# Kernel optimization log

Hardware: AMD Instinct MI355X
Metric: run time of the kernel (lower is better)

## Reference

```python
import jax, jax.numpy as jnp
import numpy as np

B, N, C_IN = 32, 4096, 32
C_OUT = 64
K = 5            # poly_degree
P = 4            # pooling_size
NNZ = 65536      # N * avg_degree(16)


def setup_inputs() -> dict:
    key = jax.random.key(0)
    ks = jax.random.split(key, 6)
    x = jax.random.normal(ks[0], (B, N, C_IN), dtype=jnp.float32)
    # scale edge values so the Chebyshev recursion stays numerically bounded
    edge_val = jax.random.normal(ks[1], (NNZ,), dtype=jnp.float32) * 0.05
    weight = jax.random.normal(ks[2], (K * C_IN, C_OUT), dtype=jnp.float32) * 0.1
    bias = jax.random.normal(ks[3], (1, 1, C_OUT), dtype=jnp.float32) * 0.1
    edge_row = jax.random.randint(ks[4], (NNZ,), 0, N, dtype=jnp.int32)
    edge_col = jax.random.randint(ks[5], (NNZ,), 0, N, dtype=jnp.int32)
    return {"x": x, "edge_val": edge_val, "weight": weight, "bias": bias,
            "edge_row": edge_row, "edge_col": edge_col}


def reference(x, edge_val, weight, bias, edge_row, edge_col):
    b, n, c = x.shape
    out_f = weight.shape[1]
    k_deg = weight.shape[0] // c

    def spmm(v):  # sparse (COO) L @ v, v: [n, c*b]
        gathered = v[edge_col] * edge_val[:, None]          # [nnz, c*b]
        return jax.ops.segment_sum(gathered, edge_row, num_segments=n)

    # x0: [n, c*b]
    x0 = jnp.transpose(x, (1, 2, 0)).reshape(n, c * b)
    x_list = [x0]
    if k_deg > 1:
        x1 = spmm(x0)
        x_list.append(x1)
    for _ in range(2, k_deg):
        x2 = 2.0 * spmm(x1) - x0
        x_list.append(x2)
        x0, x1 = x1, x2

    xs = jnp.stack(x_list, axis=0)                          # [K, n, c, b] after reshape
    xs = xs.reshape(k_deg, n, c, b)
    xs = jnp.transpose(xs, (3, 1, 2, 0))                    # [b, n, c, K]
    xs = xs.reshape(b * n, c * k_deg)
    y = (xs @ weight).reshape(b, n, out_f)                  # dense GEMM

    y = jax.nn.relu(y + bias)                               # bias + ReLU

    if P > 1:  # max pool of size P over node dim
        y = y.reshape(b, n // P, P, out_f).max(axis=2)
    return y
```

## Files before the change

kernel.cpp:

```cpp
#include <hip/hip_runtime.h>
#include <hip/hip_bf16.h>

#define BATCH 32
#define NNODE 4096
#define CIN 32
#define COUT 64
#define KDEG 5
#define POOL 4
#define NNZ_E 65536
#define BC (BATCH * CIN)
#define TBF ((size_t)NNODE * BC)
#define NSLICE 8

typedef short s16x8 __attribute__((ext_vector_type(8)));
typedef float f32x4 __attribute__((ext_vector_type(4)));
typedef unsigned long long u64;

__device__ __forceinline__ unsigned short f2bf(float f) {
    union { float f; unsigned int u; } v; v.f = f;
    unsigned int u = v.u;
    u += 0x7fffu + ((u >> 16) & 1u);
    return (unsigned short)(u >> 16);
}
__device__ __forceinline__ float bf2f(unsigned short b) {
    union { float f; unsigned int u; } v; v.u = ((unsigned int)b) << 16;
    return v.f;
}
__device__ __forceinline__ u64 pack4(float a, float b, float c, float d) {
    return (u64)f2bf(a) | ((u64)f2bf(b) << 16) | ((u64)f2bf(c) << 32) | ((u64)f2bf(d) << 48);
}


__global__ void prep_kernel(const float* __restrict__ x, unsigned short* __restrict__ t0,
                            const int* __restrict__ erow, int* __restrict__ cnt,
                            const float* __restrict__ W, unsigned short* __restrict__ WB) {
    int idx = blockIdx.x * 256 + threadIdx.x;
    int n   = idx >> 8;
    int rem = idx & 255;
    int b   = rem >> 3;
    int c4  = rem & 7;
    float4 v = ((const float4*)x)[(b * NNODE + n) * 8 + c4];
    ((u64*)t0)[idx] = pack4(v.x, v.y, v.z, v.w);

    if (idx < NNZ_E) atomicAdd(&cnt[erow[idx]], 1);

    if (idx < KDEG * COUT * CIN) {
        int c = idx & 31;
        int rest = idx >> 5;
        int o = rest & 63;
        int k = rest >> 6;
        WB[idx] = f2bf(W[(c * KDEG + k) * COUT + o]);
    }
}


__global__ void scan_kernel(const int* __restrict__ cnt, int* __restrict__ row_start,
                            int* __restrict__ cursor) {
    __shared__ int sums[256];
    int tid = threadIdx.x;
    int local[16];
    int s = 0;
#pragma unroll
    for (int i = 0; i < 16; i++) { local[i] = cnt[tid * 16 + i]; s += local[i]; }
    sums[tid] = s;
    __syncthreads();
    for (int off = 1; off < 256; off <<= 1) {
        int v = 0;
        if (tid >= off) v = sums[tid - off];
        __syncthreads();
        if (tid >= off) sums[tid] += v;
        __syncthreads();
    }
    int base = sums[tid] - s;
    int run = base;
#pragma unroll
    for (int i = 0; i < 16; i++) {
        int r = tid * 16 + i;
        row_start[r] = run;
        cursor[r] = run;
        run += local[i];
    }
    if (tid == 255) row_start[NNODE] = sums[255];
}


__global__ void scatter_kernel(const int* __restrict__ erow, const int* __restrict__ ecol,
                               const float* __restrict__ eval, int* __restrict__ cursor,
                               int2* __restrict__ es) {
    int e = blockIdx.x * blockDim.x + threadIdx.x;
    if (e < NNZ_E) {
        int pos = atomicAdd(&cursor[erow[e]], 1);
        es[pos] = make_int2(ecol[e], __float_as_int(eval[e]));
    }
}


__global__ __launch_bounds__(256) void spmm_cheb_slice_kernel(
        const unsigned short* __restrict__ in, const unsigned short* __restrict__ sub,
        unsigned short* __restrict__ out, float scale, int has_sub,
        const int* __restrict__ row_start, const int2* __restrict__ es) {
    int bx    = blockIdx.x;
    int slice = bx & 7;
    int rg    = bx >> 3;
    int wave  = threadIdx.x >> 6;
    int lane  = threadIdx.x & 63;
    int r     = rg * 4 + wave;
    int ep    = lane >> 5;
    int c     = lane & 31;
    int sc    = slice * 32 + c;

    const u64* in8 = (const u64*)in;
    int beg = row_start[r], end = row_start[r + 1];

    float4 a0 = make_float4(0.f, 0.f, 0.f, 0.f);
    float4 a1 = a0, a2 = a0, a3 = a0;

    for (int base = beg + ep; base < end; base += 8) {
        float vv[4];
        u64   xx[4];
#pragma unroll
        for (int j = 0; j < 4; j++) {
            int idx = base + 2 * j;
            int src = idx < end ? idx : beg;
            int2 e = es[src];
            vv[j] = idx < end ? __int_as_float(e.y) : 0.f;
            xx[j] = in8[(size_t)e.x * 256 + sc];
        }
        a0.x += vv[0] * bf2f((unsigned short)xx[0]);
        a0.y += vv[0] * bf2f((unsigned short)(xx[0] >> 16));
        a0.z += vv[0] * bf2f((unsigned short)(xx[0] >> 32));
        a0.w += vv[0] * bf2f((unsigned short)(xx[0] >> 48));
        a1.x += vv[1] * bf2f((unsigned short)xx[1]);
        a1.y += vv[1] * bf2f((unsigned short)(xx[1] >> 16));
        a1.z += vv[1] * bf2f((unsigned short)(xx[1] >> 32));
        a1.w += vv[1] * bf2f((unsigned short)(xx[1] >> 48));
        a2.x += vv[2] * bf2f((unsigned short)xx[2]);
        a2.y += vv[2] * bf2f((unsigned short)(xx[2] >> 16));
        a2.z += vv[2] * bf2f((unsigned short)(xx[2] >> 32));
        a2.w += vv[2] * bf2f((unsigned short)(xx[2] >> 48));
        a3.x += vv[3] * bf2f((unsigned short)xx[3]);
        a3.y += vv[3] * bf2f((unsigned short)(xx[3] >> 16));
        a3.z += vv[3] * bf2f((unsigned short)(xx[3] >> 32));
        a3.w += vv[3] * bf2f((unsigned short)(xx[3] >> 48));
    }

    float4 acc;
    acc.x = (a0.x + a1.x) + (a2.x + a3.x);
    acc.y = (a0.y + a1.y) + (a2.y + a3.y);
    acc.z = (a0.z + a1.z) + (a2.z + a3.z);
    acc.w = (a0.w + a1.w) + (a2.w + a3.w);

    acc.x += __shfl_xor(acc.x, 32);
    acc.y += __shfl_xor(acc.y, 32);
    acc.z += __shfl_xor(acc.z, 32);
    acc.w += __shfl_xor(acc.w, 32);

    if (ep == 0) {
        size_t oi = (size_t)r * 256 + sc;
        float r0, r1, r2, r3;
        if (has_sub) {
            u64 sv = __builtin_nontemporal_load((const u64*)sub + oi);
            r0 = scale * acc.x - bf2f((unsigned short)sv);
            r1 = scale * acc.y - bf2f((unsigned short)(sv >> 16));
            r2 = scale * acc.z - bf2f((unsigned short)(sv >> 32));
            r3 = scale * acc.w - bf2f((unsigned short)(sv >> 48));
        } else {
            r0 = acc.x; r1 = acc.y; r2 = acc.z; r3 = acc.w;
        }
        ((u64*)out)[oi] = pack4(r0, r1, r2, r3);
    }
}


__global__ __launch_bounds__(256) void gemm_mfma_pool_kernel(
        const unsigned short* __restrict__ tbase, const unsigned short* __restrict__ WB,
        const float* __restrict__ bias, float* __restrict__ out) {
    int gtid = blockIdx.x * 256 + threadIdx.x;
    int lane = threadIdx.x & 63;
    int wid  = gtid >> 6;
    int b    = wid >> 8;
    int n0   = (wid & 255) << 4;
    int m    = lane & 15;
    int q    = lane >> 4;

    f32x4 acc[4] = {{0.f,0.f,0.f,0.f},{0.f,0.f,0.f,0.f},
                    {0.f,0.f,0.f,0.f},{0.f,0.f,0.f,0.f}};

    const unsigned short* abase = tbase + (size_t)(n0 + m) * BC + b * CIN + q * 8;
    const unsigned short* wbase = WB + m * 32 + q * 8;

#pragma unroll
    for (int k = 0; k < KDEG; k++) {
        s16x8 a = *(const s16x8*)(abase + (size_t)k * TBF);
#pragma unroll
        for (int ot = 0; ot < 4; ot++) {
            s16x8 bf = *(const s16x8*)(wbase + ((k * 64) + ot * 16) * 32);
            acc[ot] = __builtin_amdgcn_mfma_f32_16x16x32_bf16(a, bf, acc[ot], 0, 0, 0);
        }
    }

    size_t orow = ((size_t)b * (NNODE / POOL) + (n0 >> 2) + q) * COUT;
#pragma unroll
    for (int ot = 0; ot < 4; ot++) {
        float bi = bias[ot * 16 + m];
        float r0 = acc[ot][0] + bi; r0 = r0 > 0.f ? r0 : 0.f;
        float r1 = acc[ot][1] + bi; r1 = r1 > 0.f ? r1 : 0.f;
        float r2 = acc[ot][2] + bi; r2 = r2 > 0.f ? r2 : 0.f;
        float r3 = acc[ot][3] + bi; r3 = r3 > 0.f ? r3 : 0.f;
        float mx = r0 > r1 ? r0 : r1;
        mx = mx > r2 ? mx : r2;
        mx = mx > r3 ? mx : r3;
        out[orow + ot * 16 + m] = mx;
    }
}


extern "C" void kernel_launch(void* const* d_in, const int* in_sizes, int n_in,
                              void* d_out, int out_size, void* d_ws, size_t ws_size,
                              hipStream_t stream) {
    const float* x    = (const float*)d_in[0];
    const float* eval = (const float*)d_in[1];
    const float* W    = (const float*)d_in[2];
    const float* bias = (const float*)d_in[3];
    const int*   erow = (const int*)d_in[4];
    const int*   ecol = (const int*)d_in[5];
    float* out = (float*)d_out;

    char* base = (char*)d_ws;
    unsigned short* tb = (unsigned short*)base;
    unsigned short* t0 = tb;
    unsigned short* t1 = tb + 1 * TBF;
    unsigned short* t2 = tb + 2 * TBF;
    unsigned short* t3 = tb + 3 * TBF;
    unsigned short* t4 = tb + 4 * TBF;

    size_t off = 5 * TBF * sizeof(unsigned short);
    int2* es       = (int2*)(base + off);  off += (size_t)NNZ_E * sizeof(int2);
    int* cnt       = (int*)(base + off);   off += (size_t)NNODE * sizeof(int);
    int* row_start = (int*)(base + off);   off += (size_t)(NNODE + 1) * sizeof(int);
    int* cursor    = (int*)(base + off);   off += (size_t)NNODE * sizeof(int);
    off = (off + 63) & ~(size_t)63;
    unsigned short* WB = (unsigned short*)(base + off);

    hipMemsetAsync(cnt, 0, NNODE * sizeof(int), stream);
    prep_kernel<<<TBF / 4 / 256, 256, 0, stream>>>(x, t0, erow, cnt, W, WB);
    scan_kernel<<<1, 256, 0, stream>>>(cnt, row_start, cursor);
    scatter_kernel<<<NNZ_E / 256, 256, 0, stream>>>(erow, ecol, eval, cursor, es);

    spmm_cheb_slice_kernel<<<NNODE * 2, 256, 0, stream>>>(t0, nullptr, t1, 1.0f, 0,
                                                          row_start, es);
    spmm_cheb_slice_kernel<<<NNODE * 2, 256, 0, stream>>>(t1, t0, t2, 2.0f, 1,
                                                          row_start, es);
    spmm_cheb_slice_kernel<<<NNODE * 2, 256, 0, stream>>>(t2, t1, t3, 2.0f, 1,
                                                          row_start, es);
    spmm_cheb_slice_kernel<<<NNODE * 2, 256, 0, stream>>>(t3, t2, t4, 2.0f, 1,
                                                          row_start, es);

    gemm_mfma_pool_kernel<<<(BATCH * (NNODE / 16) * 64) / 256, 256, 0, stream>>>(
        tb, WB, bias, out);
}
```

Measured before the change: 191.5 us.

## Fuse Chebyshev SpMM levels into cooperative kernel with per-slice barriers and ELL buckets

Replaces the count/scan/scatter CSR build with fixed-capacity per-row buckets (64 slots) filled directly in the prep kernel. This removes the scan and scatter launches. The four SpMM levels now run inside one persistent cooperative kernel. It synchronises with per-column-slice atomic barriers instead of separate kernel launches, and falls back to per-level launches if the cooperative launch fails. The trade-off is that rows with more than 64 edges would be silently truncated, and edge order within a row becomes nondeterministic. Spin barriers add some risk if the occupancy query is wrong.

```diff
diff --git a/kernel.cpp b/kernel.cpp
--- a/kernel.cpp
+++ b/kernel.cpp
@@ -1,5 +1,4 @@
 #include <hip/hip_runtime.h>
-#include <hip/hip_bf16.h>
 
 #define BATCH 32
 #define NNODE 4096
@@ -10,7 +9,7 @@
 #define NNZ_E 65536
 #define BC (BATCH * CIN)
 #define TBF ((size_t)NNODE * BC)
-#define NSLICE 8
+#define CAP 64
 
 typedef short s16x8 __attribute__((ext_vector_type(8)));
 typedef float f32x4 __attribute__((ext_vector_type(4)));
@@ -31,9 +30,11 @@
 }
 
 
-__global__ void prep_kernel(const float* __restrict__ x, unsigned short* __restrict__ t0,
-                            const int* __restrict__ erow, int* __restrict__ cnt,
-                            const float* __restrict__ W, unsigned short* __restrict__ WB) {
+__global__ void prep2_kernel(const float* __restrict__ x, unsigned short* __restrict__ t0,
+                             const int* __restrict__ erow, const int* __restrict__ ecol,
+                             const float* __restrict__ eval,
+                             int* __restrict__ cnt, int2* __restrict__ es,
+                             const float* __restrict__ W, unsigned short* __restrict__ WB) {
     int idx = blockIdx.x * 256 + threadIdx.x;
     int n   = idx >> 8;
     int rem = idx & 255;
@@ -42,7 +43,12 @@
     float4 v = ((const float4*)x)[(b * NNODE + n) * 8 + c4];
     ((u64*)t0)[idx] = pack4(v.x, v.y, v.z, v.w);
 
-    if (idx < NNZ_E) atomicAdd(&cnt[erow[idx]], 1);
+    if (idx < NNZ_E) {
+        int r = erow[idx];
+        int pos = atomicAdd(&cnt[r], 1);
+        if (pos < CAP)
+            es[(r << 6) + pos] = make_int2(ecol[idx], __float_as_int(eval[idx]));
+    }
 
     if (idx < KDEG * COUT * CIN) {
         int c = idx & 31;
@@ -54,63 +60,22 @@
 }
 
 
-__global__ void scan_kernel(const int* __restrict__ cnt, int* __restrict__ row_start,
-                            int* __restrict__ cursor) {
-    __shared__ int sums[256];
-    int tid = threadIdx.x;
-    int local[16];
-    int s = 0;
-#pragma unroll
-    for (int i = 0; i < 16; i++) { local[i] = cnt[tid * 16 + i]; s += local[i]; }
-    sums[tid] = s;
-    __syncthreads();
-    for (int off = 1; off < 256; off <<= 1) {
-        int v = 0;
-        if (tid >= off) v = sums[tid - off];
-        __syncthreads();
-        if (tid >= off) sums[tid] += v;
-        __syncthreads();
-    }
-    int base = sums[tid] - s;
-    int run = base;
-#pragma unroll
-    for (int i = 0; i < 16; i++) {
-        int r = tid * 16 + i;
-        row_start[r] = run;
-        cursor[r] = run;
-        run += local[i];
-    }
-    if (tid == 255) row_start[NNODE] = sums[255];
-}
-
-
-__global__ void scatter_kernel(const int* __restrict__ erow, const int* __restrict__ ecol,
-                               const float* __restrict__ eval, int* __restrict__ cursor,
-                               int2* __restrict__ es) {
-    int e = blockIdx.x * blockDim.x + threadIdx.x;
-    if (e < NNZ_E) {
-        int pos = atomicAdd(&cursor[erow[e]], 1);
-        es[pos] = make_int2(ecol[e], __float_as_int(eval[e]));
-    }
-}
-
-
-__global__ __launch_bounds__(256) void spmm_cheb_slice_kernel(
-        const unsigned short* __restrict__ in, const unsigned short* __restrict__ sub,
-        unsigned short* __restrict__ out, float scale, int has_sub,
-        const int* __restrict__ row_start, const int2* __restrict__ es) {
-    int bx    = blockIdx.x;
-    int slice = bx & 7;
-    int rg    = bx >> 3;
-    int wave  = threadIdx.x >> 6;
-    int lane  = threadIdx.x & 63;
+__device__ __forceinline__ void spmm_vb(
+        const unsigned short* in, const unsigned short* sub,
+        unsigned short* out, float scale, int has_sub,
+        const int* cnt, const int2* es, int vb, int tid) {
+    int wave = tid >> 6;
+    int lane = tid & 63;
+    int ep   = lane >> 5;
+    int c    = lane & 31;
+    int slice = vb & 7;
+    int rg    = vb >> 3;
     int r     = rg * 4 + wave;
-    int ep    = lane >> 5;
-    int c     = lane & 31;
     int sc    = slice * 32 + c;
 
     const u64* in8 = (const u64*)in;
-    int beg = row_start[r], end = row_start[r + 1];
+    int deg = cnt[r]; deg = deg > CAP ? CAP : deg;
+    int beg = r << 6, end = beg + deg;
 
     float4 a0 = make_float4(0.f, 0.f, 0.f, 0.f);
     float4 a1 = a0, a2 = a0, a3 = a0;
@@ -172,6 +137,52 @@
 }
 
 
+__device__ __forceinline__ void slice_barrier(int* ctr, int expect) {
+    __syncthreads();
+    if (threadIdx.x == 0) {
+        __hip_atomic_fetch_add(ctr, 1, __ATOMIC_RELEASE, __HIP_MEMORY_SCOPE_AGENT);
+        while (__hip_atomic_load(ctr, __ATOMIC_RELAXED, __HIP_MEMORY_SCOPE_AGENT) < expect)
+            __builtin_amdgcn_s_sleep(2);
+    }
+    __syncthreads();
+}
+
+
+__global__ __launch_bounds__(256, 8) void spmm4_coop(
+        unsigned short* __restrict__ tb, const int* __restrict__ cnt,
+        const int2* __restrict__ es, int* __restrict__ bar) {
+    int bid = blockIdx.x, tid = threadIdx.x, nb = gridDim.x;
+    int expect = nb >> 3;
+    int slice = bid & 7;
+
+    const unsigned short* t0 = tb;
+    unsigned short* t1 = tb + 1 * TBF;
+    unsigned short* t2 = tb + 2 * TBF;
+    unsigned short* t3 = tb + 3 * TBF;
+    unsigned short* t4 = tb + 4 * TBF;
+
+    for (int vb = bid; vb < NNODE * 2; vb += nb)
+        spmm_vb(t0, nullptr, t1, 1.0f, 0, cnt, es, vb, tid);
+    slice_barrier(&bar[0 * 8 + slice], expect);
+    for (int vb = bid; vb < NNODE * 2; vb += nb)
+        spmm_vb(t1, t0, t2, 2.0f, 1, cnt, es, vb, tid);
+    slice_barrier(&bar[1 * 8 + slice], expect);
+    for (int vb = bid; vb < NNODE * 2; vb += nb)
+        spmm_vb(t2, t1, t3, 2.0f, 1, cnt, es, vb, tid);
+    slice_barrier(&bar[2 * 8 + slice], expect);
+    for (int vb = bid; vb < NNODE * 2; vb += nb)
+        spmm_vb(t3, t2, t4, 2.0f, 1, cnt, es, vb, tid);
+}
+
+
+__global__ __launch_bounds__(256) void spmm_lvl_kernel(
+        const unsigned short* __restrict__ in, const unsigned short* __restrict__ sub,
+        unsigned short* __restrict__ out, float scale, int has_sub,
+        const int* __restrict__ cnt, const int2* __restrict__ es) {
+    spmm_vb(in, sub, out, scale, has_sub, cnt, es, blockIdx.x, threadIdx.x);
+}
+
+
 __global__ __launch_bounds__(256) void gemm_mfma_pool_kernel(
         const unsigned short* __restrict__ tbase, const unsigned short* __restrict__ WB,
         const float* __restrict__ bias, float* __restrict__ out) {
@@ -235,26 +246,41 @@
     unsigned short* t4 = tb + 4 * TBF;
 
     size_t off = 5 * TBF * sizeof(unsigned short);
-    int2* es       = (int2*)(base + off);  off += (size_t)NNZ_E * sizeof(int2);
-    int* cnt       = (int*)(base + off);   off += (size_t)NNODE * sizeof(int);
-    int* row_start = (int*)(base + off);   off += (size_t)(NNODE + 1) * sizeof(int);
-    int* cursor    = (int*)(base + off);   off += (size_t)NNODE * sizeof(int);
+    int2* es = (int2*)(base + off);  off += (size_t)NNODE * CAP * sizeof(int2);
+    int* cnt = (int*)(base + off);   off += (size_t)NNODE * sizeof(int);
+    int* bar = (int*)(base + off);   off += 32 * sizeof(int);
     off = (off + 63) & ~(size_t)63;
     unsigned short* WB = (unsigned short*)(base + off);
 
-    hipMemsetAsync(cnt, 0, NNODE * sizeof(int), stream);
-    prep_kernel<<<TBF / 4 / 256, 256, 0, stream>>>(x, t0, erow, cnt, W, WB);
-    scan_kernel<<<1, 256, 0, stream>>>(cnt, row_start, cursor);
-    scatter_kernel<<<NNZ_E / 256, 256, 0, stream>>>(erow, ecol, eval, cursor, es);
-
-    spmm_cheb_slice_kernel<<<NNODE * 2, 256, 0, stream>>>(t0, nullptr, t1, 1.0f, 0,
-                                                          row_start, es);
-    spmm_cheb_slice_kernel<<<NNODE * 2, 256, 0, stream>>>(t1, t0, t2, 2.0f, 1,
-                                                          row_start, es);
-    spmm_cheb_slice_kernel<<<NNODE * 2, 256, 0, stream>>>(t2, t1, t3, 2.0f, 1,
-                                                          row_start, es);
-    spmm_cheb_slice_kernel<<<NNODE * 2, 256, 0, stream>>>(t3, t2, t4, 2.0f, 1,
-                                                          row_start, es);
+    hipMemsetAsync(cnt, 0, (NNODE + 32) * sizeof(int), stream);
+
+    prep2_kernel<<<TBF / 4 / 256, 256, 0, stream>>>(x, t0, erow, ecol, eval,
+                                                    cnt, es, W, WB);
+
+    static int coop_grid = -1;
+    if (coop_grid < 0) {
+        int per_cu = 0;
+        hipError_t qe = hipOccupancyMaxActiveBlocksPerMultiprocessor(
+            &per_cu, spmm4_coop, 256, 0);
+        int cap = (qe == hipSuccess) ? per_cu * 256 : 0;
+        coop_grid = cap >= 2048 ? 2048 : (cap >= 1024 ? 1024 : 0);
+    }
+
+    bool coop_ok = false;
+    if (coop_grid > 0) {
+        void* kargs[] = { (void*)&tb, (void*)&cnt, (void*)&es, (void*)&bar };
+        hipError_t err = hipLaunchCooperativeKernel((const void*)spmm4_coop,
+                                                    dim3(coop_grid), dim3(256),
+                                                    kargs, 0, stream);
+        coop_ok = (err == hipSuccess);
+        if (!coop_ok) coop_grid = 0;
+    }
+    if (!coop_ok) {
+        spmm_lvl_kernel<<<NNODE * 2, 256, 0, stream>>>(t0, nullptr, t1, 1.0f, 0, cnt, es);
+        spmm_lvl_kernel<<<NNODE * 2, 256, 0, stream>>>(t1, t0, t2, 2.0f, 1, cnt, es);
+        spmm_lvl_kernel<<<NNODE * 2, 256, 0, stream>>>(t2, t1, t3, 2.0f, 1, cnt, es);
+        spmm_lvl_kernel<<<NNODE * 2, 256, 0, stream>>>(t3, t2, t4, 2.0f, 1, cnt, es);
+    }
 
     gemm_mfma_pool_kernel<<<(BATCH * (NNODE / 16) * 64) / 256, 256, 0, stream>>>(
         tb, WB, bias, out);
```

New measurement: 540.8 us. 2.82x slower.
